# Performance work log

Hardware: AMD Instinct MI355X
Metric: run time of the kernel (lower is better)

## Reference

```python
import jax, jax.numpy as jnp
import numpy as np

B, S, D = 4, 2048, 512
H = 8
DK = D // H
F = 2048  # filter_size
K = 9     # kernel_size
PAD = (K - 1) // 2
EPS = 1e-5


def layer_norm(x, gamma, beta):
    mu = jnp.mean(x, axis=-1, keepdims=True)
    var = jnp.var(x, axis=-1, keepdims=True)
    return (x - mu) * jax.lax.rsqrt(var + EPS) * gamma + beta


def conv1d(x_bcs, w_oik, b):
    # x: (B, C, S), w: (O, I, K) torch Conv1d layout, SAME padding
    y = jax.lax.conv_general_dilated(
        x_bcs, w_oik, window_strides=(1,), padding=[(PAD, PAD)],
        dimension_numbers=("NCH", "OIH", "NCH"))
    return y + b[None, :, None]


def setup_inputs() -> dict:
    key = jax.random.key(0)
    ks = jax.random.split(key, 16)
    g = lambda k, shp: (jax.random.normal(k, shp, dtype=jnp.float32) * 0.02)
    return {
        "src": jax.random.normal(ks[0], (B, S, D), dtype=jnp.float32),
        "src_mask": jnp.ones((B, 1, S), dtype=bool),
        "wq": g(ks[1], (D, D)), "bq": jnp.zeros((D,), jnp.float32),
        "wk": g(ks[2], (D, D)), "bk": jnp.zeros((D,), jnp.float32),
        "wv": g(ks[3], (D, D)), "bv": jnp.zeros((D,), jnp.float32),
        "wo": g(ks[4], (D, D)), "bo": jnp.zeros((D,), jnp.float32),
        "conv1_w": g(ks[5], (F, D, K)), "conv1_b": jnp.zeros((F,), jnp.float32),
        "conv2_w": g(ks[6], (D, F, K)), "conv2_b": jnp.zeros((D,), jnp.float32),
        "g1": jnp.ones((D,), jnp.float32), "b1": jnp.zeros((D,), jnp.float32),
        "g2": jnp.ones((D,), jnp.float32), "b2": jnp.zeros((D,), jnp.float32),
    }


def reference(src, src_mask, wq, bq, wk, bk, wv, bv, wo, bo,
              conv1_w, conv1_b, conv2_w, conv2_b, g1, b1, g2, b2):
    # ---- multi-head self attention (naive, explicit score matrix) ----
    q = (src @ wq.T + bq).reshape(B, S, H, DK).transpose(0, 2, 1, 3)  # (B,H,S,DK)
    k = (src @ wk.T + bk).reshape(B, S, H, DK).transpose(0, 2, 1, 3)
    v = (src @ wv.T + bv).reshape(B, S, H, DK).transpose(0, 2, 1, 3)
    scores = jnp.einsum("bhqd,bhkd->bhqk", q, k) / jnp.sqrt(jnp.float32(DK))
    mask4 = src_mask[:, None, :, :]  # (B,1,1,S) broadcast over heads/queries
    scores = jnp.where(mask4, scores, jnp.float32(-1e9))
    attn = jax.nn.softmax(scores, axis=-1)
    ctx = jnp.einsum("bhqk,bhkd->bhqd", attn, v)
    ctx = ctx.transpose(0, 2, 1, 3).reshape(B, S, D)
    attn_out = ctx @ wo.T + bo
    x = layer_norm(src + attn_out, g1, b1)
    # ---- conv1d FFN ----
    h = x.transpose(0, 2, 1)                       # (B, D, S)
    h = jax.nn.relu(conv1d(h, conv1_w, conv1_b))   # (B, F, S)
    h = conv1d(h, conv2_w, conv2_b)                # (B, D, S)
    ffn_out = h.transpose(0, 2, 1)
    return layer_norm(x + ffn_out, g2, b2)
```

## Files before the change

kernel.cpp:

```cpp
#include <hip/hip_runtime.h>


#define DEV __device__ __forceinline__

typedef __attribute__((ext_vector_type(8))) short bf16x8_t;
typedef __attribute__((ext_vector_type(4))) float f32x4_t;

DEV unsigned short f2bf(float f) {
  union { float f; unsigned u; } c; c.f = f;
  return (unsigned short)((c.u + 0x7fffu + ((c.u >> 16) & 1u)) >> 16);
}
DEV float bf2f(unsigned short h) {
  union { unsigned u; float f; } c; c.u = ((unsigned)h) << 16;
  return c.f;
}

DEV void stage16(const unsigned short* g, unsigned short* lds_base, int lane) {
#if __has_builtin(__builtin_amdgcn_global_load_lds)
  (void)lane;
  __builtin_amdgcn_global_load_lds(
      (const __attribute__((address_space(1))) void*)g,
      (__attribute__((address_space(3))) void*)lds_base, 16, 0, 0);
#else
  *(bf16x8_t*)(lds_base + lane * 8) = *(const bf16x8_t*)g;
#endif
}

template <int CK, int OUTMODE, int N, int K, int LDA, int LDO, int KSPLIT>
__global__ __launch_bounds__(256, 4) void gemm_bt(
    const unsigned short* __restrict__ A, const unsigned short* __restrict__ B,
    const float* __restrict__ bias, void* __restrict__ out, void* __restrict__ out2,
    long pstride) {
  __shared__ __align__(16) unsigned short As[2][128 * 32];
  __shared__ __align__(16) unsigned short Bs[2][128 * 32];
  const int tid = threadIdx.x;
  const int lane = tid & 63, wave = tid >> 6;
  const int quad = lane >> 4, l16 = lane & 15;
  const int bm = blockIdx.x << 7, bn = blockIdx.y << 7;
  const int wr = (wave >> 1) << 6, wc = (wave & 1) << 6;
  const int k0 = blockIdx.z * KSPLIT;

  f32x4_t acc[4][4];
#pragma unroll
  for (int i = 0; i < 4; i++)
#pragma unroll
    for (int j = 0; j < 4; j++) acc[i][j] = (f32x4_t){0.f, 0.f, 0.f, 0.f};

  const int srow = (wave << 4) + (lane >> 2);
  const int scol = (lane & 3) << 3;

#pragma unroll 1
  for (int kb = 0; kb < KSPLIT; kb += 64) {
    __syncthreads();
#pragma unroll
    for (int h = 0; h < 2; h++) {
      const int k = k0 + kb + (h << 5);
      int ktap, kcol;
      if (CK > 0) { ktap = k / CK; kcol = k % CK; } else { ktap = 0; kcol = k; }
#pragma unroll
      for (int i = 0; i < 2; i++) {
        const int r = (i << 6) + srow;
        const int am = bm + r;
        const int arow = (CK > 0) ? (am + ((am >> 11) << 3) + ktap) : am;
        stage16(A + (long)arow * LDA + kcol + scol, &As[h][(i << 11) + (wave << 9)], lane);
        stage16(B + (long)(bn + r) * K + k + scol, &Bs[h][(i << 11) + (wave << 9)], lane);
      }
    }
    __syncthreads();

#pragma unroll
    for (int h = 0; h < 2; h++) {
      bf16x8_t af[4], bfr[4];
#pragma unroll
      for (int t = 0; t < 4; t++)
        af[t] = *(const bf16x8_t*)&As[h][((wr + (t << 4) + l16) << 5) + (quad << 3)];
#pragma unroll
      for (int t = 0; t < 4; t++)
        bfr[t] = *(const bf16x8_t*)&Bs[h][((wc + (t << 4) + l16) << 5) + (quad << 3)];
#pragma unroll
      for (int mt = 0; mt < 4; mt++)
#pragma unroll
        for (int nt = 0; nt < 4; nt++)
          acc[mt][nt] = __builtin_amdgcn_mfma_f32_16x16x32_bf16(af[mt], bfr[nt],
                                                                acc[mt][nt], 0, 0, 0);
    }
  }

  unsigned short* po = (unsigned short*)out;
  if (OUTMODE == 3)
    po = (blockIdx.z == 3) ? (unsigned short*)out2
                           : (unsigned short*)out + (long)blockIdx.z * pstride;
  float* fo = (float*)out;
  if (OUTMODE == 1) fo = (blockIdx.z == 0) ? (float*)out : (float*)out2;

#pragma unroll
  for (int mt = 0; mt < 4; mt++)
#pragma unroll
    for (int nt = 0; nt < 4; nt++) {
      const int col = bn + wc + (nt << 4) + l16;
      float bv = 0.f;
      if (OUTMODE == 0 || OUTMODE == 2) bv = bias[col];
      if (OUTMODE == 1) bv = (blockIdx.z == 0) ? bias[col] : 0.f;
#pragma unroll
      for (int r = 0; r < 4; r++) {
        const int row = bm + wr + (mt << 4) + (quad << 2) + r;
        float v = acc[mt][nt][r] + bv;
        if (OUTMODE == 0) {
          ((unsigned short*)out)[(long)row * LDO + col] = f2bf(v);
        } else if (OUTMODE == 1) {
          fo[(long)row * LDO + col] = v;
        } else if (OUTMODE == 2) {
          v = v > 0.f ? v : 0.f;
          const int orow = row + ((row >> 11) << 3) + 4;
          ((unsigned short*)out)[(long)orow * LDO + col] = f2bf(v);
        } else {
          po[(long)row * LDO + col] = f2bf(v);
        }
      }
    }
}

__global__ __launch_bounds__(256) void transpose_v(
    const unsigned short* __restrict__ qkv16, unsigned short* __restrict__ vT) {
  __shared__ unsigned short T[64][72];
  const int tid = threadIdx.x;
  const int st = blockIdx.x, bh = blockIdx.y;
  const int b = bh >> 3, h = bh & 7;
  const long rowbase = (long)b << 11;
  const int s0 = st << 6;
  const int rr = tid >> 3, cc = (tid & 7) << 3;
#pragma unroll
  for (int p = 0; p < 2; p++) {
    const int s = (p << 5) + rr;
    bf16x8_t v = *(const bf16x8_t*)(qkv16 + (rowbase + s0 + s) * 1536 + 1024 + (h << 6) + cc);
#pragma unroll
    for (int i = 0; i < 8; i++) T[cc + i][s] = (unsigned short)v[i];
  }
  __syncthreads();
  const int dd = tid >> 3, sc = (tid & 7) << 3;
#pragma unroll
  for (int p = 0; p < 2; p++) {
    const int d = (p << 5) + dd;
    bf16x8_t o;
#pragma unroll
    for (int i = 0; i < 8; i++) o[i] = (short)T[d][sc + i];
    *(bf16x8_t*)(vT + ((long)(b * 512 + (h << 6) + d) << 11) + s0 + sc) = o;
  }
}

__global__ __launch_bounds__(256) void flash_attn(
    const unsigned short* __restrict__ q16, const unsigned short* __restrict__ k16,
    const unsigned short* __restrict__ vT, unsigned short* __restrict__ ctx16) {
  const int LDQ = 1536;
  __shared__ __align__(16) unsigned short Ks[64 * 64];
  __shared__ __align__(16) unsigned short Vt[64 * 64];
  __shared__ __align__(16) unsigned short Ps[4][16 * 80];

  const int tid = threadIdx.x;
  const int lane = tid & 63, wave = tid >> 6;
  const int quad = lane >> 4, l16 = lane & 15;
  const int qt = blockIdx.x, bh = blockIdx.y;
  const int b = bh >> 3, h = bh & 7;
  const long rowbase = (long)b << 11;
  const int hoff = h << 6;

  const long qrow = rowbase + (qt << 6) + (wave << 4) + l16;
  const bf16x8_t qa0 = *(const bf16x8_t*)(q16 + qrow * LDQ + hoff + (quad << 3));
  const bf16x8_t qa1 = *(const bf16x8_t*)(q16 + qrow * LDQ + hoff + 32 + (quad << 3));

  bf16x8_t ones;
#pragma unroll
  for (int i = 0; i < 8; i++) ones[i] = (short)0x3F80;

  f32x4_t o[4];
#pragma unroll
  for (int i = 0; i < 4; i++) o[i] = (f32x4_t){0.f, 0.f, 0.f, 0.f};
  f32x4_t l4 = {0.f, 0.f, 0.f, 0.f};

  const int srow8 = lane >> 3;
  const int scol8 = (lane & 7) << 3;
  const unsigned short* vbase = vT + ((long)(b * 512 + hoff) << 11);

  for (int kt = 0; kt < 2048; kt += 64) {
    __syncthreads();
#pragma unroll
    for (int j = 0; j < 2; j++) {
      const int kr = (wave << 4) + (j << 3);
      stage16(k16 + (rowbase + kt + kr + srow8) * LDQ + hoff + scol8, &Ks[kr << 6], lane);
      stage16(vbase + ((long)(kr + srow8) << 11) + kt + scol8, &Vt[kr << 6], lane);
    }
    __syncthreads();

    f32x4_t s[4];
#pragma unroll
    for (int t = 0; t < 4; t++) s[t] = (f32x4_t){0.f, 0.f, 0.f, 0.f};
#pragma unroll
    for (int t = 0; t < 4; t++) {
      const bf16x8_t k0 = *(const bf16x8_t*)&Ks[(((t << 4) + l16) << 6) + (quad << 3)];
      const bf16x8_t k1 = *(const bf16x8_t*)&Ks[(((t << 4) + l16) << 6) + 32 + (quad << 3)];
      s[t] = __builtin_amdgcn_mfma_f32_16x16x32_bf16(qa0, k0, s[t], 0, 0, 0);
      s[t] = __builtin_amdgcn_mfma_f32_16x16x32_bf16(qa1, k1, s[t], 0, 0, 0);
    }
#pragma unroll
    for (int r = 0; r < 4; r++)
#pragma unroll
      for (int t = 0; t < 4; t++)
        Ps[wave][((quad << 2) + r) * 80 + (t << 4) + l16] =
            f2bf(__expf(s[t][r] * 0.125f));
    const bf16x8_t pa0 = *(const bf16x8_t*)&Ps[wave][l16 * 80 + (quad << 3)];
    const bf16x8_t pa1 = *(const bf16x8_t*)&Ps[wave][l16 * 80 + 32 + (quad << 3)];
    l4 = __builtin_amdgcn_mfma_f32_16x16x32_bf16(pa0, ones, l4, 0, 0, 0);
    l4 = __builtin_amdgcn_mfma_f32_16x16x32_bf16(pa1, ones, l4, 0, 0, 0);
#pragma unroll
    for (int dt = 0; dt < 4; dt++) {
      const bf16x8_t v0 = *(const bf16x8_t*)&Vt[(((dt << 4) + l16) << 6) + (quad << 3)];
      const bf16x8_t v1 = *(const bf16x8_t*)&Vt[(((dt << 4) + l16) << 6) + 32 + (quad << 3)];
      o[dt] = __builtin_amdgcn_mfma_f32_16x16x32_bf16(pa0, v0, o[dt], 0, 0, 0);
      o[dt] = __builtin_amdgcn_mfma_f32_16x16x32_bf16(pa1, v1, o[dt], 0, 0, 0);
    }
  }

#pragma unroll
  for (int r = 0; r < 4; r++) {
    const float inv = 1.f / l4[r];
    const long orow = rowbase + (qt << 6) + (wave << 4) + (quad << 2) + r;
#pragma unroll
    for (int dt = 0; dt < 4; dt++)
      ctx16[(orow << 9) + hoff + (dt << 4) + l16] = f2bf(o[dt][r] * inv);
  }
}

__global__ __launch_bounds__(256) void ln_fused(
    const float* __restrict__ xa, const float* __restrict__ xb,
    const float* __restrict__ xc, const float* __restrict__ gamma,
    const float* __restrict__ beta, unsigned short* __restrict__ padout) {
  const int lane = threadIdx.x & 63, wave = threadIdx.x >> 6;
  const long row = ((long)blockIdx.x << 2) + wave;
  const long base = (row << 9) + (lane << 3);
  float s[8];
  {
    const float4 a0 = *(const float4*)(xa + base);
    const float4 a1 = *(const float4*)(xa + base + 4);
    const float4 b0 = *(const float4*)(xb + base);
    const float4 b1 = *(const float4*)(xb + base + 4);
    const float4 c0 = *(const float4*)(xc + base);
    const float4 c1 = *(const float4*)(xc + base + 4);
    s[0] = a0.x + b0.x + c0.x; s[1] = a0.y + b0.y + c0.y;
    s[2] = a0.z + b0.z + c0.z; s[3] = a0.w + b0.w + c0.w;
    s[4] = a1.x + b1.x + c1.x; s[5] = a1.y + b1.y + c1.y;
    s[6] = a1.z + b1.z + c1.z; s[7] = a1.w + b1.w + c1.w;
  }
  float sum = 0.f, sq = 0.f;
#pragma unroll
  for (int i = 0; i < 8; i++) { sum += s[i]; sq += s[i] * s[i]; }
#pragma unroll
  for (int d = 1; d < 64; d <<= 1) { sum += __shfl_xor(sum, d); sq += __shfl_xor(sq, d); }
  const float mean = sum * (1.f / 512.f);
  const float var = sq * (1.f / 512.f) - mean * mean;
  const float rstd = rsqrtf(var + 1e-5f);
  const int col = lane << 3;
  const long prow = row + ((row >> 11) << 3) + 4;
  bf16x8_t pv;
#pragma unroll
  for (int i = 0; i < 8; i++)
    pv[i] = (short)f2bf((s[i] - mean) * rstd * gamma[col + i] + beta[col + i]);
  *(bf16x8_t*)(padout + (prow << 9) + (lane << 3)) = pv;
}

__global__ __launch_bounds__(256) void ln2_red(
    const unsigned short* __restrict__ xpad, const unsigned short* __restrict__ pA,
    const unsigned short* __restrict__ pB, const float* __restrict__ bias,
    const float* __restrict__ gamma, const float* __restrict__ beta,
    float* __restrict__ out) {
  const int lane = threadIdx.x & 63, wave = threadIdx.x >> 6;
  const long row = ((long)blockIdx.x << 2) + wave;
  const long base = (row << 9) + (lane << 3);
  const int col = lane << 3;
  const long prow = row + ((row >> 11) << 3) + 4;
  const bf16x8_t xr = *(const bf16x8_t*)(xpad + (prow << 9) + (lane << 3));
  const bf16x8_t p0 = *(const bf16x8_t*)(pA + base);
  const bf16x8_t p1 = *(const bf16x8_t*)(pA + 4194304 + base);
  const bf16x8_t p2 = *(const bf16x8_t*)(pA + 8388608 + base);
  const bf16x8_t p3 = *(const bf16x8_t*)(pB + base);
  float s[8];
#pragma unroll
  for (int i = 0; i < 8; i++) {
    s[i] = bf2f((unsigned short)xr[i]) + bias[col + i] +
           bf2f((unsigned short)p0[i]) + bf2f((unsigned short)p1[i]) +
           bf2f((unsigned short)p2[i]) + bf2f((unsigned short)p3[i]);
  }
  float sum = 0.f, sq = 0.f;
#pragma unroll
  for (int i = 0; i < 8; i++) { sum += s[i]; sq += s[i] * s[i]; }
#pragma unroll
  for (int d = 1; d < 64; d <<= 1) { sum += __shfl_xor(sum, d); sq += __shfl_xor(sq, d); }
  const float mean = sum * (1.f / 512.f);
  const float var = sq * (1.f / 512.f) - mean * mean;
  const float rstd = rsqrtf(var + 1e-5f);
  float y[8];
#pragma unroll
  for (int i = 0; i < 8; i++) y[i] = (s[i] - mean) * rstd * gamma[col + i] + beta[col + i];
  float4 y0 = {y[0], y[1], y[2], y[3]}, y1 = {y[4], y[5], y[6], y[7]};
  *(float4*)(out + base) = y0;
  *(float4*)(out + base + 4) = y1;
}

__global__ void prep(const float* __restrict__ src, unsigned short* __restrict__ src16,
                     const float* __restrict__ wq, const float* __restrict__ wk,
                     const float* __restrict__ wv, const float* __restrict__ wo,
                     unsigned short* __restrict__ wqkv16, unsigned short* __restrict__ wo16,
                     const float* __restrict__ c1w, unsigned short* __restrict__ w1p,
                     const float* __restrict__ c2w, unsigned short* __restrict__ w2p,
                     unsigned short* __restrict__ xpad,
                     const float* __restrict__ bq, const float* __restrict__ bk,
                     const float* __restrict__ bv, float* __restrict__ bqkv) {
  const int bid = blockIdx.x, tid = threadIdx.x;
  if (bid < 4096) {
    const int i = bid * 256 + tid;
    const float4 v = ((const float4*)src)[i];
    ushort4 r; r.x = f2bf(v.x); r.y = f2bf(v.y); r.z = f2bf(v.z); r.w = f2bf(v.w);
    ((ushort4*)src16)[i] = r;
  } else if (bid < 5120) {
    const int w = (bid - 4096) >> 8;
    const int i = ((bid - 4096) & 255) * 256 + tid;
    const float* sp = (w == 0) ? wq : (w == 1) ? wk : (w == 2) ? wv : wo;
    unsigned short* dp = (w < 3) ? (wqkv16 + (w << 18)) : wo16;
    const float4 v = ((const float4*)sp)[i];
    ushort4 r; r.x = f2bf(v.x); r.y = f2bf(v.y); r.z = f2bf(v.z); r.w = f2bf(v.w);
    ((ushort4*)dp)[i] = r;
  } else if (bid < 9216) {
    const int idx = (bid - 5120) * 256 + tid;
    const int c = idx & 511, f = idx >> 9;
    float vals[9];
#pragma unroll
    for (int k = 0; k < 9; k++) vals[k] = c1w[(long)idx * 9 + k];
#pragma unroll
    for (int k = 0; k < 9; k++)
      w1p[(((long)f * 9 + k) << 9) + c] = f2bf(vals[k]);
  } else if (bid < 13312) {
    const int idx = (bid - 9216) * 256 + tid;
    const int c = idx & 2047, f = idx >> 11;
    float vals[9];
#pragma unroll
    for (int k = 0; k < 9; k++) vals[k] = c2w[(long)idx * 9 + k];
#pragma unroll
    for (int k = 0; k < 9; k++)
      w2p[(((long)f * 9 + k) << 11) + c] = f2bf(vals[k]);
  } else if (bid < 13376) {
    const int i = (bid - 13312) * 256 + tid;
    const int b = i >> 12, r = (i >> 9) & 7, c = i & 511;
    const int t = (r < 4) ? r : 2048 + r;
    xpad[((long)b * 2056 + t) * 512 + c] = 0;
  } else {
    const int i = (bid - 13376) * 256 + tid;
    bqkv[i] = (i < 512) ? bq[i] : (i < 1024) ? bk[i - 512] : bv[i - 1024];
  }
}

__global__ void zero_hpad(unsigned short* __restrict__ hpad) {
  const long j = (long)blockIdx.x * 256 + threadIdx.x;
  const int b = j >> 14, r = (j >> 11) & 7, c = j & 2047;
  const int t = (r < 4) ? r : 2048 + r;
  hpad[((long)b * 2056 + t) * 2048 + c] = 0;
}

extern "C" void kernel_launch(void* const* d_in, const int* in_sizes, int n_in,
                              void* d_out, int out_size, void* d_ws, size_t ws_size,
                              hipStream_t stream) {
  (void)in_sizes; (void)n_in; (void)out_size; (void)ws_size;
  const float* src = (const float*)d_in[0];
  const float* wq = (const float*)d_in[2];  const float* bq = (const float*)d_in[3];
  const float* wk = (const float*)d_in[4];  const float* bk = (const float*)d_in[5];
  const float* wv = (const float*)d_in[6];  const float* bv = (const float*)d_in[7];
  const float* wo = (const float*)d_in[8];  const float* bo = (const float*)d_in[9];
  const float* c1w = (const float*)d_in[10]; const float* c1b = (const float*)d_in[11];
  const float* c2w = (const float*)d_in[12]; const float* c2b = (const float*)d_in[13];
  const float* g1 = (const float*)d_in[14]; const float* b1 = (const float*)d_in[15];
  const float* g2 = (const float*)d_in[16]; const float* b2 = (const float*)d_in[17];
  float* out = (float*)d_out;

  char* ws = (char*)d_ws;
  unsigned short* src16  = (unsigned short*)(ws + 0);
  unsigned short* vT     = (unsigned short*)(ws + 0);
  unsigned short* wqkv16 = (unsigned short*)(ws + 8388608);
  unsigned short* wo16   = wqkv16 + 786432;
  unsigned short* qkv16  = (unsigned short*)(ws + 10485760);
  float* proj1           = (float*)(ws + 10485760);
  unsigned short* ctx16  = (unsigned short*)(ws + 35651584);
  float* bqkv            = (float*)(ws + 35651584);
  float* attn_out        = (float*)(ws + 44040192);
  unsigned short* xpad   = (unsigned short*)(ws + 77594624);
  unsigned short* w1p    = (unsigned short*)(ws + 86016000);
  unsigned short* w2p    = (unsigned short*)(ws + 104890368);
  unsigned short* hpad   = (unsigned short*)(ws + 0);
  unsigned short* pA     = (unsigned short*)(ws + 35651584);
  unsigned short* pB     = (unsigned short*)(ws + 60817408);

  prep<<<13382, 256, 0, stream>>>(src, src16, wq, wk, wv, wo, wqkv16, wo16,
                                  c1w, w1p, c2w, w2p, xpad, bq, bk, bv, bqkv);

  gemm_bt<0, 0, 1536, 512, 512, 1536, 512><<<dim3(64, 12, 1), 256, 0, stream>>>(
      src16, wqkv16, bqkv, qkv16, nullptr, 0);

  transpose_v<<<dim3(32, 32), 256, 0, stream>>>(qkv16, vT);
  flash_attn<<<dim3(32, 32), 256, 0, stream>>>(qkv16, qkv16 + 512, vT, ctx16);

  gemm_bt<0, 1, 512, 512, 512, 512, 256><<<dim3(64, 4, 2), 256, 0, stream>>>(
      ctx16, wo16, bo, attn_out, proj1, 0);

  ln_fused<<<2048, 256, 0, stream>>>(src, attn_out, proj1, g1, b1, xpad);

  zero_hpad<<<256, 256, 0, stream>>>(hpad);

  gemm_bt<512, 2, 2048, 4608, 512, 2048, 4608><<<dim3(64, 16, 1), 256, 0, stream>>>(
      xpad, w1p, c1b, hpad, nullptr, 0);

  gemm_bt<2048, 3, 512, 18432, 2048, 512, 4608><<<dim3(64, 4, 4), 256, 0, stream>>>(
      hpad, w2p, nullptr, pA, pB, 4194304);

  ln2_red<<<2048, 256, 0, stream>>>(xpad, pA, pB, c2b, g2, b2, out);
}
```

Measured before the change: 642.2 us.

## Fuse V transpose into QKV GEMM epilogue and process two query tiles per wave

The QKV projection GEMM gains an output mode that writes Q/K packed with stride 1024 and writes V directly in transposed (B*D, S) layout, removing the separate transpose_v kernel and its extra read/write of V. Flash attention now handles 128 query rows per block (32 per wave), reusing each K/V tile loaded into LDS for two query sub-tiles. This halves the number of K/V loads per query and uses half as many blocks. The P conversion to bf16 is switched to truncation instead of round-to-nearest, which slightly lowers precision. Doubling the accumulators raises register pressure.

```diff
diff --git a/kernel.cpp b/kernel.cpp
--- a/kernel.cpp
+++ b/kernel.cpp
@@ -84,6 +84,34 @@
           acc[mt][nt] = __builtin_amdgcn_mfma_f32_16x16x32_bf16(af[mt], bfr[nt],
                                                                 acc[mt][nt], 0, 0, 0);
     }
+  }
+
+  if (OUTMODE == 4) {
+    const bool isqk = (blockIdx.y < 8);
+#pragma unroll
+    for (int mt = 0; mt < 4; mt++)
+#pragma unroll
+      for (int nt = 0; nt < 4; nt++) {
+        const int col = bn + wc + (nt << 4) + l16;
+        const float bv = bias[col];
+        const int rowb = bm + wr + (mt << 4) + (quad << 2);
+        if (isqk) {
+#pragma unroll
+          for (int r = 0; r < 4; r++)
+            ((unsigned short*)out)[(long)(rowb + r) * 1024 + col] =
+                f2bf(acc[mt][nt][r] + bv);
+        } else {
+          ushort4 pk;
+          pk.x = f2bf(acc[mt][nt][0] + bv);
+          pk.y = f2bf(acc[mt][nt][1] + bv);
+          pk.z = f2bf(acc[mt][nt][2] + bv);
+          pk.w = f2bf(acc[mt][nt][3] + bv);
+          const int vcol = col - 1024;
+          const int bb = rowb >> 11, s = rowb & 2047;
+          *(ushort4*)((unsigned short*)out2 + ((long)(bb * 512 + vcol) << 11) + s) = pk;
+        }
+      }
+    return;
   }
 
   unsigned short* po = (unsigned short*)out;
@@ -120,41 +148,12 @@
     }
 }
 
-__global__ __launch_bounds__(256) void transpose_v(
-    const unsigned short* __restrict__ qkv16, unsigned short* __restrict__ vT) {
-  __shared__ unsigned short T[64][72];
-  const int tid = threadIdx.x;
-  const int st = blockIdx.x, bh = blockIdx.y;
-  const int b = bh >> 3, h = bh & 7;
-  const long rowbase = (long)b << 11;
-  const int s0 = st << 6;
-  const int rr = tid >> 3, cc = (tid & 7) << 3;
-#pragma unroll
-  for (int p = 0; p < 2; p++) {
-    const int s = (p << 5) + rr;
-    bf16x8_t v = *(const bf16x8_t*)(qkv16 + (rowbase + s0 + s) * 1536 + 1024 + (h << 6) + cc);
-#pragma unroll
-    for (int i = 0; i < 8; i++) T[cc + i][s] = (unsigned short)v[i];
-  }
-  __syncthreads();
-  const int dd = tid >> 3, sc = (tid & 7) << 3;
-#pragma unroll
-  for (int p = 0; p < 2; p++) {
-    const int d = (p << 5) + dd;
-    bf16x8_t o;
-#pragma unroll
-    for (int i = 0; i < 8; i++) o[i] = (short)T[d][sc + i];
-    *(bf16x8_t*)(vT + ((long)(b * 512 + (h << 6) + d) << 11) + s0 + sc) = o;
-  }
-}
-
 __global__ __launch_bounds__(256) void flash_attn(
-    const unsigned short* __restrict__ q16, const unsigned short* __restrict__ k16,
-    const unsigned short* __restrict__ vT, unsigned short* __restrict__ ctx16) {
-  const int LDQ = 1536;
+    const unsigned short* __restrict__ qk16, const unsigned short* __restrict__ vT,
+    unsigned short* __restrict__ ctx16) {
   __shared__ __align__(16) unsigned short Ks[64 * 64];
   __shared__ __align__(16) unsigned short Vt[64 * 64];
-  __shared__ __align__(16) unsigned short Ps[4][16 * 80];
+  __shared__ __align__(16) unsigned short Ps[4][2][16 * 80];
 
   const int tid = threadIdx.x;
   const int lane = tid & 63, wave = tid >> 6;
@@ -163,22 +162,29 @@
   const int b = bh >> 3, h = bh & 7;
   const long rowbase = (long)b << 11;
   const int hoff = h << 6;
-
-  const long qrow = rowbase + (qt << 6) + (wave << 4) + l16;
-  const bf16x8_t qa0 = *(const bf16x8_t*)(q16 + qrow * LDQ + hoff + (quad << 3));
-  const bf16x8_t qa1 = *(const bf16x8_t*)(q16 + qrow * LDQ + hoff + 32 + (quad << 3));
-
+  const int qbase = (qt << 7) + (wave << 5);
+
+  bf16x8_t qa[2][2];
+#pragma unroll
+  for (int hh = 0; hh < 2; hh++) {
+    const long qrow = rowbase + qbase + (hh << 4) + l16;
+    qa[hh][0] = *(const bf16x8_t*)(qk16 + (qrow << 10) + hoff + (quad << 3));
+    qa[hh][1] = *(const bf16x8_t*)(qk16 + (qrow << 10) + hoff + 32 + (quad << 3));
+  }
   bf16x8_t ones;
 #pragma unroll
   for (int i = 0; i < 8; i++) ones[i] = (short)0x3F80;
 
-  f32x4_t o[4];
-#pragma unroll
-  for (int i = 0; i < 4; i++) o[i] = (f32x4_t){0.f, 0.f, 0.f, 0.f};
-  f32x4_t l4 = {0.f, 0.f, 0.f, 0.f};
+  f32x4_t o[2][4];
+#pragma unroll
+  for (int hh = 0; hh < 2; hh++)
+#pragma unroll
+    for (int i = 0; i < 4; i++) o[hh][i] = (f32x4_t){0.f, 0.f, 0.f, 0.f};
+  f32x4_t l4[2] = {{0.f, 0.f, 0.f, 0.f}, {0.f, 0.f, 0.f, 0.f}};
 
   const int srow8 = lane >> 3;
   const int scol8 = (lane & 7) << 3;
+  const unsigned short* kbase = qk16 + 512;
   const unsigned short* vbase = vT + ((long)(b * 512 + hoff) << 11);
 
   for (int kt = 0; kt < 2048; kt += 64) {
@@ -186,48 +192,68 @@
 #pragma unroll
     for (int j = 0; j < 2; j++) {
       const int kr = (wave << 4) + (j << 3);
-      stage16(k16 + (rowbase + kt + kr + srow8) * LDQ + hoff + scol8, &Ks[kr << 6], lane);
+      stage16(kbase + ((rowbase + kt + kr + srow8) << 10) + hoff + scol8,
+              &Ks[kr << 6], lane);
       stage16(vbase + ((long)(kr + srow8) << 11) + kt + scol8, &Vt[kr << 6], lane);
     }
     __syncthreads();
 
-    f32x4_t s[4];
-#pragma unroll
-    for (int t = 0; t < 4; t++) s[t] = (f32x4_t){0.f, 0.f, 0.f, 0.f};
+    bf16x8_t kf[4][2];
 #pragma unroll
     for (int t = 0; t < 4; t++) {
-      const bf16x8_t k0 = *(const bf16x8_t*)&Ks[(((t << 4) + l16) << 6) + (quad << 3)];
-      const bf16x8_t k1 = *(const bf16x8_t*)&Ks[(((t << 4) + l16) << 6) + 32 + (quad << 3)];
-      s[t] = __builtin_amdgcn_mfma_f32_16x16x32_bf16(qa0, k0, s[t], 0, 0, 0);
-      s[t] = __builtin_amdgcn_mfma_f32_16x16x32_bf16(qa1, k1, s[t], 0, 0, 0);
-    }
-#pragma unroll
-    for (int r = 0; r < 4; r++)
-#pragma unroll
-      for (int t = 0; t < 4; t++)
-        Ps[wave][((quad << 2) + r) * 80 + (t << 4) + l16] =
-            f2bf(__expf(s[t][r] * 0.125f));
-    const bf16x8_t pa0 = *(const bf16x8_t*)&Ps[wave][l16 * 80 + (quad << 3)];
-    const bf16x8_t pa1 = *(const bf16x8_t*)&Ps[wave][l16 * 80 + 32 + (quad << 3)];
-    l4 = __builtin_amdgcn_mfma_f32_16x16x32_bf16(pa0, ones, l4, 0, 0, 0);
-    l4 = __builtin_amdgcn_mfma_f32_16x16x32_bf16(pa1, ones, l4, 0, 0, 0);
-#pragma unroll
-    for (int dt = 0; dt < 4; dt++) {
-      const bf16x8_t v0 = *(const bf16x8_t*)&Vt[(((dt << 4) + l16) << 6) + (quad << 3)];
-      const bf16x8_t v1 = *(const bf16x8_t*)&Vt[(((dt << 4) + l16) << 6) + 32 + (quad << 3)];
-      o[dt] = __builtin_amdgcn_mfma_f32_16x16x32_bf16(pa0, v0, o[dt], 0, 0, 0);
-      o[dt] = __builtin_amdgcn_mfma_f32_16x16x32_bf16(pa1, v1, o[dt], 0, 0, 0);
-    }
-  }
-
-#pragma unroll
-  for (int r = 0; r < 4; r++) {
-    const float inv = 1.f / l4[r];
-    const long orow = rowbase + (qt << 6) + (wave << 4) + (quad << 2) + r;
-#pragma unroll
-    for (int dt = 0; dt < 4; dt++)
-      ctx16[(orow << 9) + hoff + (dt << 4) + l16] = f2bf(o[dt][r] * inv);
-  }
+      kf[t][0] = *(const bf16x8_t*)&Ks[(((t << 4) + l16) << 6) + (quad << 3)];
+      kf[t][1] = *(const bf16x8_t*)&Ks[(((t << 4) + l16) << 6) + 32 + (quad << 3)];
+    }
+#pragma unroll
+    for (int hh = 0; hh < 2; hh++) {
+      f32x4_t s[4];
+#pragma unroll
+      for (int t = 0; t < 4; t++) s[t] = (f32x4_t){0.f, 0.f, 0.f, 0.f};
+#pragma unroll
+      for (int t = 0; t < 4; t++) {
+        s[t] = __builtin_amdgcn_mfma_f32_16x16x32_bf16(qa[hh][0], kf[t][0], s[t], 0, 0, 0);
+        s[t] = __builtin_amdgcn_mfma_f32_16x16x32_bf16(qa[hh][1], kf[t][1], s[t], 0, 0, 0);
+      }
+#pragma unroll
+      for (int r = 0; r < 4; r++)
+#pragma unroll
+        for (int t = 0; t < 4; t++) {
+          union { float f; unsigned u; } cv;
+          cv.f = __expf(s[t][r] * 0.125f);
+          Ps[wave][hh][((quad << 2) + r) * 80 + (t << 4) + l16] =
+              (unsigned short)(cv.u >> 16);
+        }
+    }
+    bf16x8_t vf[4][2];
+#pragma unroll
+    for (int t = 0; t < 4; t++) {
+      vf[t][0] = *(const bf16x8_t*)&Vt[(((t << 4) + l16) << 6) + (quad << 3)];
+      vf[t][1] = *(const bf16x8_t*)&Vt[(((t << 4) + l16) << 6) + 32 + (quad << 3)];
+    }
+#pragma unroll
+    for (int hh = 0; hh < 2; hh++) {
+      const bf16x8_t pa0 = *(const bf16x8_t*)&Ps[wave][hh][l16 * 80 + (quad << 3)];
+      const bf16x8_t pa1 = *(const bf16x8_t*)&Ps[wave][hh][l16 * 80 + 32 + (quad << 3)];
+      l4[hh] = __builtin_amdgcn_mfma_f32_16x16x32_bf16(pa0, ones, l4[hh], 0, 0, 0);
+      l4[hh] = __builtin_amdgcn_mfma_f32_16x16x32_bf16(pa1, ones, l4[hh], 0, 0, 0);
+#pragma unroll
+      for (int dt = 0; dt < 4; dt++) {
+        o[hh][dt] = __builtin_amdgcn_mfma_f32_16x16x32_bf16(pa0, vf[dt][0], o[hh][dt], 0, 0, 0);
+        o[hh][dt] = __builtin_amdgcn_mfma_f32_16x16x32_bf16(pa1, vf[dt][1], o[hh][dt], 0, 0, 0);
+      }
+    }
+  }
+
+#pragma unroll
+  for (int hh = 0; hh < 2; hh++)
+#pragma unroll
+    for (int r = 0; r < 4; r++) {
+      const float inv = 1.f / l4[hh][r];
+      const long orow = rowbase + qbase + (hh << 4) + (quad << 2) + r;
+#pragma unroll
+      for (int dt = 0; dt < 4; dt++)
+        ctx16[(orow << 9) + hoff + (dt << 4) + l16] = f2bf(o[hh][dt][r] * inv);
+    }
 }
 
 __global__ __launch_bounds__(256) void ln_fused(
@@ -381,11 +407,11 @@
 
   char* ws = (char*)d_ws;
   unsigned short* src16  = (unsigned short*)(ws + 0);
-  unsigned short* vT     = (unsigned short*)(ws + 0);
   unsigned short* wqkv16 = (unsigned short*)(ws + 8388608);
   unsigned short* wo16   = wqkv16 + 786432;
-  unsigned short* qkv16  = (unsigned short*)(ws + 10485760);
+  unsigned short* qk16   = (unsigned short*)(ws + 10485760);
   float* proj1           = (float*)(ws + 10485760);
+  unsigned short* vT     = (unsigned short*)(ws + 27262976);
   unsigned short* ctx16  = (unsigned short*)(ws + 35651584);
   float* bqkv            = (float*)(ws + 35651584);
   float* attn_out        = (float*)(ws + 44040192);
@@ -399,11 +425,10 @@
   prep<<<13382, 256, 0, stream>>>(src, src16, wq, wk, wv, wo, wqkv16, wo16,
                                   c1w, w1p, c2w, w2p, xpad, bq, bk, bv, bqkv);
 
-  gemm_bt<0, 0, 1536, 512, 512, 1536, 512><<<dim3(64, 12, 1), 256, 0, stream>>>(
-      src16, wqkv16, bqkv, qkv16, nullptr, 0);
-
-  transpose_v<<<dim3(32, 32), 256, 0, stream>>>(qkv16, vT);
-  flash_attn<<<dim3(32, 32), 256, 0, stream>>>(qkv16, qkv16 + 512, vT, ctx16);
+  gemm_bt<0, 4, 1536, 512, 512, 1024, 512><<<dim3(64, 12, 1), 256, 0, stream>>>(
+      src16, wqkv16, bqkv, qk16, vT, 0);
+
+  flash_attn<<<dim3(16, 32), 256, 0, stream>>>(qk16, vT, ctx16);
 
   gemm_bt<0, 1, 512, 512, 512, 512, 256><<<dim3(64, 4, 2), 256, 0, stream>>>(
       ctx16, wo16, bo, attn_out, proj1, 0);
```

New measurement: 607.2 us. 1.06x faster.
